# Kernel tuning notes

Hardware: AMD Instinct MI355X
Metric: run time of the kernel (lower is better)

Reference implementation:

```python
import jax, jax.numpy as jnp
import numpy as np

D_MODEL, D_STATE, EXPAND = 1024, 128, 2
E = D_MODEL * EXPAND          # 2048
N = D_STATE                   # 128
H = 1
P = E
TD = D_STATE // 2             # 64
Z_DIM = E + E + N + N + H + H + TD + H  # 4369
EPS = 1e-05
B_SZ, L = 4, 2048


def setup_inputs() -> dict:
    key = jax.random.key(0)
    ks = jax.random.split(key, 6)
    u = jax.random.normal(ks[0], (B_SZ, L, D_MODEL), dtype=jnp.float32)
    W_in = jax.random.normal(ks[1], (Z_DIM, D_MODEL), dtype=jnp.float32) * 0.02
    W_out = jax.random.normal(ks[2], (D_MODEL, E), dtype=jnp.float32) * 0.02
    w_normB = jnp.ones((N,), jnp.float32)
    w_normC = jnp.ones((N,), jnp.float32)
    B_bias = jnp.ones((N,), jnp.float32)
    C_bias = jnp.ones((N,), jnp.float32)
    # dt_bias buffer: dt_i ~ logU(0.001, 0.1); dt_bias = dt_i + log(-expm1(-dt_i))
    dt_i = jnp.exp(jax.random.uniform(ks[3], (H,)) * (np.log(0.1) - np.log(0.001)) + np.log(0.001))
    dt_i = jnp.clip(dt_i, 1e-4, None)
    dt_bias = dt_i + jnp.log(-jnp.expm1(-dt_i))
    A_log = jnp.full((H,), np.log(0.5), jnp.float32)
    return {"u": u, "W_in": W_in, "w_normB": w_normB, "w_normC": w_normC,
            "B_bias": B_bias, "C_bias": C_bias, "dt_bias": dt_bias,
            "A_log": A_log, "W_out": W_out}


def _rms(x, w):
    return x * jax.lax.rsqrt(jnp.mean(x * x, axis=-1, keepdims=True) + EPS) * w


def _rope(x, ang):
    half = x.shape[-1] // 2
    x1, x2 = x[..., :half], x[..., half:]
    c, s = jnp.cos(ang), jnp.sin(ang)
    return jnp.concatenate([x1 * c - x2 * s, x1 * s + x2 * c], axis=-1)


def reference(u, W_in, w_normB, w_normC, B_bias, C_bias, dt_bias, A_log, W_out):
    Bb, Ls, _ = u.shape
    z = u @ W_in.T  # [B, L, Z_DIM]
    o = 0
    def take(n):
        nonlocal o
        r = z[..., o:o + n]; o += n; return r
    x = jax.nn.silu(take(E))
    gate = jax.nn.silu(take(E))
    B_ = take(N)
    C_ = take(N)
    dt_ = take(H)
    A_ = take(H)
    th = take(TD)
    lam_ = take(H)

    dt = jax.nn.softplus(dt_ + dt_bias)          # [B, L, H]
    A = -jax.nn.softplus(A_ + A_log)             # [B, L, H]
    lam = jax.nn.sigmoid(lam_)                   # [B, L, H]
    alpha = jnp.exp(dt * A)                      # [B, L, H]

    B_ = _rms(B_, w_normB) + B_bias
    C_ = _rms(C_, w_normC) + C_bias
    ca = jnp.cumsum(jnp.mean(dt, axis=-1, keepdims=True) * th, axis=1)  # [B, L, TD]
    B_ = _rope(B_, ca)
    C_ = _rope(C_, ca)

    xh = x.reshape(Bb, Ls, H, P)
    xp = jnp.concatenate([jnp.zeros_like(xh[:, :1]), xh[:, :-1]], axis=1)  # roll + zero t=0
    lh = lam[..., None]
    xt = lh * xh + (1.0 - lh) * alpha[..., None] * xp  # [B, L, H, P]

    # fallback SSM: per-channel mean drive, per-head scalar A (mean over batch+time)
    u_mean = jnp.mean(xt, axis=-1)               # [B, L, H]
    A_bar = jnp.mean(A, axis=(0, 1))             # [H]
    dA = jnp.exp(dt * A_bar)                     # [B, L, H]
    dBu = dt[..., None] * B_[:, :, None, :] * u_mean[..., None]  # [B, L, H, N]

    def step(state, xs):
        dA_t, dBu_t, C_t = xs                    # [B,H], [B,H,N], [B,N]
        state = dA_t[..., None] * state + dBu_t  # [B, H, N]
        y_t = jnp.einsum('bhn,bn->bh', state, C_t)
        return state, y_t

    state0 = jnp.zeros((Bb, H, N), dtype=xt.dtype)
    _, ys = jax.lax.scan(step, state0,
                         (jnp.moveaxis(dA, 1, 0), jnp.moveaxis(dBu, 1, 0), jnp.moveaxis(C_, 1, 0)))
    outs = jnp.moveaxis(ys, 0, 1)                # [B, L, H]
    y = jnp.broadcast_to(outs, (Bb, Ls, E))      # H=1 expanded to E
    return (y * gate) @ W_out.T
```

## Files before the change

### kernel.cpp

```cpp
#include <hip/hip_runtime.h>
#include <cstdint>
#include <cstddef>

typedef __bf16 bf16_t;
typedef bf16_t bf16x8 __attribute__((ext_vector_type(8)));
typedef bf16_t bf16x4 __attribute__((ext_vector_type(4)));
typedef float f32x4 __attribute__((ext_vector_type(4)));

#define B_SZ    4
#define LSEQ    2048
#define DMODEL  1024
#define EDIM    2048
#define ZDIM    4419
#define ZPAD    4608
#define ROWS    (B_SZ*LSEQ)
#define EPSV    1e-5f

#define LDU     1088
#define LDG     2112

#define SCHUNK  128
#define SCLEN   (LSEQ/SCHUNK)
#define RCH     128
#define RCLEN   (LSEQ/RCH)

__device__ __forceinline__ float softplus_f(float x){
  return fmaxf(x, 0.f) + log1pf(expf(-fabsf(x)));
}
__device__ __forceinline__ float sigmoid_f(float x){ return 1.f/(1.f+expf(-x)); }
__device__ __forceinline__ float silu_f(float x){ return x/(1.f+expf(-x)); }

__device__ __forceinline__ void gload_lds16(const void* g, void* l){
  __builtin_amdgcn_global_load_lds(
      (const __attribute__((address_space(1))) void*)g,
      (__attribute__((address_space(3))) void*)l, 16, 0, 0);
}

__device__ __forceinline__ float blockReduce128(float v, float* red, int t){
  red[t] = v; __syncthreads();
  #pragma unroll
  for (int off = 64; off > 0; off >>= 1){
    if (t < off) red[t] += red[t+off];
    __syncthreads();
  }
  float r = red[0];
  __syncthreads();
  return r;
}

__global__ __launch_bounds__(256) void prep_kernel(
    const float4* __restrict__ u4, const float4* __restrict__ win4,
    const float4* __restrict__ wout4,
    bf16_t* __restrict__ ubf, bf16_t* __restrict__ winSh, bf16_t* __restrict__ woutSh,
    float* __restrict__ Asum, float* __restrict__ xraw)
{
  size_t i = (size_t)blockIdx.x*256 + threadIdx.x;
  if (i == 0) Asum[0] = 0.f;
  if (i < ROWS) xraw[i] = 0.f;
  const size_t NU4 = (size_t)ROWS*DMODEL/4;
  const size_t NW4 = (size_t)ZPAD*DMODEL/4;
  const size_t NO4 = (size_t)DMODEL*EDIM/4;
  if (i < NU4){
    float4 v = u4[i];
    size_t e = i*4, row = e>>10, col = e&1023;
    bf16x4 o = { (bf16_t)v.x, (bf16_t)v.y, (bf16_t)v.z, (bf16_t)v.w };
    *(bf16x4*)&ubf[row*LDU + col] = o;
    return;
  }
  i -= NU4;
  if (i < NW4){
    size_t e = i*4, row = e>>10, k = e&1023;
    bf16x4 o;
    if (row < (size_t)ZDIM){
      float4 v = win4[i];
      o = bf16x4{ (bf16_t)v.x, (bf16_t)v.y, (bf16_t)v.z, (bf16_t)v.w };
    } else {
      o = bf16x4{ (bf16_t)0.f, (bf16_t)0.f, (bf16_t)0.f, (bf16_t)0.f };
    }
    int ntile = (int)(row>>4), colf = (int)(row&15);
    int kt = (int)(k>>5), koct = (int)((k>>3)&3), ko = (int)(k&7);
    size_t off = (((size_t)ntile*32 + kt)<<9) + (koct<<7) + (colf<<3) + ko;
    *(bf16x4*)&winSh[off] = o;
    return;
  }
  i -= NW4;
  if (i < NO4){
    float4 v = wout4[i];
    size_t e = i*4, row = e>>11, k = e&2047;
    bf16x4 o = { (bf16_t)v.x, (bf16_t)v.y, (bf16_t)v.z, (bf16_t)v.w };
    int ntile = (int)(row>>4), colf = (int)(row&15);
    int kt = (int)(k>>5), koct = (int)((k>>3)&3), ko = (int)(k&7);
    size_t off = (((size_t)ntile*64 + kt)<<9) + (koct<<7) + (colf<<3) + ko;
    *(bf16x4*)&woutSh[off] = o;
  }
}

template<int LDA_, int NKT, int NT, int NXT, int MODE>
__global__ __launch_bounds__(256, 2) void gemmV_kernel(
    const bf16_t* __restrict__ A0, const bf16_t* __restrict__ Bsh,
    float* __restrict__ xraw, bf16_t* __restrict__ o_g, float* __restrict__ o_z,
    const float* __restrict__ scale, float* __restrict__ o_f)
{
  __shared__ __align__(16) bf16_t lds[8192];

  const int tid = threadIdx.x;
  const int wid = tid>>6, lane = tid&63;
  const int wr = wid>>1, wc = wid&1;
  const int lr = lane&15, hi = lane>>4;

  constexpr int MB = ROWS/128;
  constexpr int NWG = (MODE==0) ? NXT*MB : NXT*MB*2;
  const int id = blockIdx.x;
  const int rid = (id & 7)*(NWG/8) + (id>>3);
  int bx, by, kz = 0;
  if (MODE == 0){ bx = rid % NXT; by = rid / NXT; }
  else { kz = rid / (NXT*MB); int r2 = rid % (NXT*MB); bx = r2 % NXT; by = r2 / NXT; }
  const int m0 = by*128, n0 = bx*256;
  const int kt0 = kz*32;

  f32x4 acc[4][8] = {};

  const bf16_t* pA0; const bf16_t* pA1;
  int dA0, dA1;
  {
    int c0 = tid,      r0 = c0>>2, d0 = c0&3, g0 = (d0 - (r0>>1)) & 3;
    int c1 = 256+tid,  r1 = c1>>2, d1 = c1&3, g1 = (d1 - (r1>>1)) & 3;
    pA0 = A0 + (size_t)kz*1024 + (size_t)(m0+r0)*LDA_ + g0*8;
    pA1 = A0 + (size_t)kz*1024 + (size_t)(m0+r1)*LDA_ + g1*8;
    dA0 = c0*8; dA1 = c1*8;
  }
  int aoff[4];
  {
    int R0 = wr*64 + lr;
    int cA = (hi + (R0>>1)) & 3;
    #pragma unroll
    for (int m = 0; m < 4; ++m) aoff[m] = (R0 + 16*m)*32 + cA*8;
  }
  const bf16_t* bB0 = Bsh + (((size_t)((n0>>4) + wc*8)*NKT + kt0)<<9) + lane*8;
  int koff = 0;

  bf16x8 bA[8], bB[8], af[4];

  gload_lds16(pA0, &lds[dA0]); pA0 += 32;
  gload_lds16(pA1, &lds[dA1]); pA1 += 32;
  #pragma unroll
  for (int n = 0; n < 8; ++n)
    bA[n] = *(const bf16x8*)(bB0 + (size_t)n*(NKT*512) + koff);
  koff += 512;
  asm volatile("s_waitcnt vmcnt(8)" ::: "memory");
  __builtin_amdgcn_s_barrier();

  #pragma unroll 1
  for (int t2 = 0; t2 < NT/2; ++t2){
    {
      #pragma unroll
      for (int m = 0; m < 4; ++m) af[m] = *(const bf16x8*)&lds[aoff[m]];
      gload_lds16(pA0, &lds[4096 + dA0]); pA0 += 32;
      gload_lds16(pA1, &lds[4096 + dA1]); pA1 += 32;
      #pragma unroll
      for (int n = 0; n < 8; ++n)
        bB[n] = *(const bf16x8*)(bB0 + (size_t)n*(NKT*512) + koff);
      koff += 512;
      #pragma unroll
      for (int m = 0; m < 4; ++m)
        #pragma unroll
        for (int n = 0; n < 8; ++n)
          acc[m][n] = __builtin_amdgcn_mfma_f32_16x16x32_bf16(af[m], bA[n], acc[m][n], 0,0,0);
      asm volatile("s_waitcnt vmcnt(8)" ::: "memory");
      __builtin_amdgcn_s_barrier();
    }
    {
      #pragma unroll
      for (int m = 0; m < 4; ++m) af[m] = *(const bf16x8*)&lds[4096 + aoff[m]];
      const bool pf = (t2 < NT/2 - 1);
      if (pf){
        gload_lds16(pA0, &lds[dA0]); pA0 += 32;
        gload_lds16(pA1, &lds[dA1]); pA1 += 32;
        #pragma unroll
        for (int n = 0; n < 8; ++n)
          bA[n] = *(const bf16x8*)(bB0 + (size_t)n*(NKT*512) + koff);
        koff += 512;
      }
      #pragma unroll
      for (int m = 0; m < 4; ++m)
        #pragma unroll
        for (int n = 0; n < 8; ++n)
          acc[m][n] = __builtin_amdgcn_mfma_f32_16x16x32_bf16(af[m], bB[n], acc[m][n], 0,0,0);
      if (pf) { asm volatile("s_waitcnt vmcnt(8)" ::: "memory"); }
      else    { asm volatile("s_waitcnt vmcnt(0)" ::: "memory"); }
      __builtin_amdgcn_s_barrier();
    }
  }

  if (MODE == 0 && n0 < 2048){
    #pragma unroll
    for (int m = 0; m < 4; ++m){
      #pragma unroll
      for (int i = 0; i < 4; ++i){
        float p = 0.f;
        #pragma unroll
        for (int n = 0; n < 8; ++n) p += silu_f(acc[m][n][i]);
        p += __shfl_xor(p, 8); p += __shfl_xor(p, 4);
        p += __shfl_xor(p, 2); p += __shfl_xor(p, 1);
        if (lr == 0){
          int r = m0 + wr*64 + m*16 + (hi<<2) + i;
          atomicAdd(xraw + r, p);
        }
      }
    }
  } else if (MODE == 0){
    #pragma unroll
    for (int m = 0; m < 4; ++m){
      int rowb = m0 + wr*64 + m*16 + (hi<<2);
      #pragma unroll
      for (int n = 0; n < 8; ++n){
        int col = n0 + wc*128 + n*16 + lr;
        #pragma unroll
        for (int i = 0; i < 4; ++i){
          int r = rowb + i;
          float v = acc[m][n][i];
          if (col < 4096)      o_g[(size_t)r*LDG + (col-2048)] = (bf16_t)silu_f(v);
          else if (col < 4480) o_z[(size_t)r*384 + (col-4096)] = v;
        }
      }
    }
  } else {
    #pragma unroll
    for (int m = 0; m < 4; ++m){
      int rowb = m0 + wr*64 + m*16 + (hi<<2);
      #pragma unroll
      for (int i = 0; i < 4; ++i){
        int r = rowb + i;
        float s = scale[r];
        #pragma unroll
        for (int n = 0; n < 8; ++n){
          int col = n0 + wc*128 + n*16 + lr;
          atomicAdd(o_f + (size_t)r*DMODEL + col, acc[m][n][i]*s);
        }
      }
    }
  }
}

__global__ __launch_bounds__(128) void fuse_kernel(
    const float* __restrict__ xraw, const float* __restrict__ zs,
    const float* __restrict__ wnB, const float* __restrict__ wnC,
    const float* __restrict__ Bb, const float* __restrict__ Cb,
    const float* __restrict__ dtb, const float* __restrict__ Alog,
    float* __restrict__ Bn, float* __restrict__ Cn, float* __restrict__ dtth,
    float* __restrict__ dts, float* __restrict__ alphas, float* __restrict__ lams,
    float* __restrict__ xbar, float* Asum)
{
  __shared__ float red[128];
  int r = blockIdx.x, t = threadIdx.x;
  const float* zr = zs + (size_t)r*384;
  float bv = zr[t], cv = zr[128+t];
  float b2 = blockReduce128(bv*bv, red, t);
  float c2 = blockReduce128(cv*cv, red, t);
  float rb = rsqrtf(b2*(1.f/128.f) + EPSV);
  float rc = rsqrtf(c2*(1.f/128.f) + EPSV);
  Bn[(size_t)r*128 + t] = bv*rb*wnB[t] + Bb[t];
  Cn[(size_t)r*128 + t] = cv*rc*wnC[t] + Cb[t];

  float dt = softplus_f(zr[256] + dtb[0]);
  if (t < 64) dtth[(size_t)r*64 + t] = dt * zr[258+t];
  if (t == 0){
    float Av  = -softplus_f(zr[257] + Alog[0]);
    float lam = sigmoid_f(zr[322]);
    dts[r]    = dt;
    alphas[r] = expf(dt*Av);
    lams[r]   = lam;
    xbar[r]   = xraw[r] * (1.f/2048.f);
    atomicAdd(Asum, Av);
  }
}

__global__ __launch_bounds__(64) void rope_sum_kernel(
    const float* __restrict__ dtth, float* __restrict__ csum)
{
  int b  = blockIdx.x >> 7;
  int ch = blockIdx.x & 127;
  int d  = threadIdx.x;
  const float* base = dtth + ((size_t)b*LSEQ + (size_t)ch*RCLEN)*64 + d;
  float s = 0.f;
  #pragma unroll
  for (int i = 0; i < RCLEN; ++i) s += base[(size_t)i*64];
  csum[((size_t)b*RCH + ch)*64 + d] = s;
}

__global__ __launch_bounds__(64) void rope_prefix_kernel(float* __restrict__ csum)
{
  int b = blockIdx.x, d = threadIdx.x;
  float s = 0.f;
  for (int c = 0; c < RCH; ++c){
    size_t idx = ((size_t)b*RCH + c)*64 + d;
    float v = csum[idx]; csum[idx] = s; s += v;
  }
}

__global__ __launch_bounds__(64) void rope_apply_kernel(
    const float* __restrict__ dtth, const float* __restrict__ csum,
    float* __restrict__ Bn, float* __restrict__ Cn)
{
  int b  = blockIdx.x >> 7;
  int ch = blockIdx.x & 127;
  int d  = threadIdx.x;
  float ca = csum[((size_t)b*RCH + ch)*64 + d];
  int l0 = ch*RCLEN;
  const float* base = dtth + ((size_t)b*LSEQ)*64 + d;
  for (int l = l0; l < l0 + RCLEN; ++l){
    ca += base[(size_t)l*64];
    float sn, cs;
    sincosf(ca, &sn, &cs);
    size_t ro = ((size_t)b*LSEQ + l)*128;
    float b1 = Bn[ro+d], b2v = Bn[ro+64+d];
    Bn[ro+d]    = b1*cs - b2v*sn;
    Bn[ro+64+d] = b1*sn + b2v*cs;
    float c1 = Cn[ro+d], c2v = Cn[ro+64+d];
    Cn[ro+d]    = c1*cs - c2v*sn;
    Cn[ro+64+d] = c1*sn + c2v*cs;
  }
}

__global__ __launch_bounds__(64) void scan_local_kernel(
    const float* __restrict__ dts, const float* __restrict__ alphas,
    const float* __restrict__ lams, const float* __restrict__ xbar,
    const float* __restrict__ Asum,
    const float* __restrict__ Bn, const float* __restrict__ Cn,
    float* __restrict__ ylocal, float* __restrict__ Pfix,
    float* __restrict__ Sfin, float* __restrict__ Dch)
{
  int b  = blockIdx.x / SCHUNK;
  int ch = blockIdx.x % SCHUNK;
  int n  = threadIdx.x;
  float Abar = Asum[0] * (1.f/(float)ROWS);
  float s1 = 0.f, s2 = 0.f, P = 1.f;
  int l0 = ch*SCLEN;
  #pragma unroll
  for (int i = 0; i < SCLEN; ++i){
    int l = l0 + i;
    size_t r = (size_t)b*LSEQ + l;
    float dt = dts[r], lam = lams[r], al = alphas[r], xb = xbar[r];
    float xp = (l > 0) ? xbar[r-1] : 0.f;
    float um = lam*xb + (1.f-lam)*al*xp;
    float dA = expf(dt*Abar);
    float coef = dt*um;
    size_t ro = r*128;
    s1 = dA*s1 + coef*Bn[ro+n];
    s2 = dA*s2 + coef*Bn[ro+64+n];
    P *= dA;
    float p = s1*Cn[ro+n] + s2*Cn[ro+64+n];
    #pragma unroll
    for (int off = 32; off > 0; off >>= 1) p += __shfl_down(p, off);
    if (n == 0){ ylocal[r] = p; Pfix[r] = P; }
  }
  size_t so = ((size_t)b*SCHUNK + ch)*128;
  Sfin[so + n]      = s1;
  Sfin[so + 64 + n] = s2;
  if (n == 0) Dch[b*SCHUNK + ch] = P;
}

__global__ __launch_bounds__(128) void scan_carry_kernel(
    const float* __restrict__ Sfin, const float* __restrict__ Dch,
    float* __restrict__ Sin)
{
  int b = blockIdx.x;
  int n = threadIdx.x;
  float s = 0.f;
  for (int c = 0; c < SCHUNK; ++c){
    size_t so = ((size_t)b*SCHUNK + c)*128;
    Sin[so + n] = s;
    s = Dch[b*SCHUNK + c]*s + Sfin[so + n];
  }
}

__global__ __launch_bounds__(256) void scan_fix_kernel(
    const float* __restrict__ Cn, const float* __restrict__ Sin,
    const float* __restrict__ ylocal, const float* __restrict__ Pfix,
    float* __restrict__ outsv)
{
  int r = blockIdx.x*4 + (threadIdx.x>>6);
  int n = threadIdx.x & 63;
  int b  = r / LSEQ;
  int ch = (r % LSEQ) / SCLEN;
  const float* si = Sin + ((size_t)b*SCHUNK + ch)*128;
  size_t ro = (size_t)r*128;
  float p = Cn[ro+n]*si[n] + Cn[ro+64+n]*si[64+n];
  #pragma unroll
  for (int off = 32; off > 0; off >>= 1) p += __shfl_down(p, off);
  if (n == 0) outsv[r] = ylocal[r] + Pfix[r]*p;
}

extern "C" void kernel_launch(void* const* d_in, const int* in_sizes, int n_in,
                              void* d_out, int out_size, void* d_ws, size_t ws_size,
                              hipStream_t stream)
{
  const float* u    = (const float*)d_in[0];
  const float* W_in = (const float*)d_in[1];
  const float* wnB  = (const float*)d_in[2];
  const float* wnC  = (const float*)d_in[3];
  const float* Bb   = (const float*)d_in[4];
  const float* Cb   = (const float*)d_in[5];
  const float* dtb  = (const float*)d_in[6];
  const float* Alog = (const float*)d_in[7];
  const float* Wout = (const float*)d_in[8];
  float* out = (float*)d_out;
  char* ws = (char*)d_ws;

  constexpr size_t OFF_ASUM = 0;
  constexpr size_t OFF_UBF  = 256;
  constexpr size_t SZ_UBF   = (size_t)ROWS*LDU*2;
  constexpr size_t OFF_WIN  = OFF_UBF + SZ_UBF;
  constexpr size_t SZ_WIN   = (size_t)ZPAD*LDU*2;
  constexpr size_t OFF_WOUT = OFF_WIN + SZ_WIN;
  constexpr size_t SZ_WOUT  = (size_t)DMODEL*LDG*2;
  constexpr size_t OFF_G    = OFF_WOUT + SZ_WOUT;
  constexpr size_t SZ_G     = (size_t)ROWS*LDG*2;
  constexpr size_t OFF_ZS   = OFF_G + SZ_G;
  constexpr size_t SZ_ZS    = (size_t)ROWS*384*4;
  constexpr size_t OFF_BN   = OFF_ZS + SZ_ZS;
  constexpr size_t SZ_BN    = (size_t)ROWS*128*4;
  constexpr size_t OFF_CN   = OFF_BN + SZ_BN;
  constexpr size_t OFF_DTTH = OFF_CN + SZ_BN;
  constexpr size_t SZ_DTTH  = (size_t)ROWS*64*4;
  constexpr size_t OFF_XRAW = OFF_DTTH + SZ_DTTH;
  constexpr size_t OFF_DT   = OFF_XRAW + (size_t)ROWS*4;
  constexpr size_t OFF_AL   = OFF_DT  + (size_t)ROWS*4;
  constexpr size_t OFF_LAM  = OFF_AL  + (size_t)ROWS*4;
  constexpr size_t OFF_XB   = OFF_LAM + (size_t)ROWS*4;
  constexpr size_t OFF_OUTS = OFF_XB  + (size_t)ROWS*4;
  constexpr size_t OFF_YLOC = OFF_OUTS + (size_t)ROWS*4;
  constexpr size_t OFF_PFIX = OFF_YLOC + (size_t)ROWS*4;
  constexpr size_t OFF_SFIN = OFF_PFIX + (size_t)ROWS*4;
  constexpr size_t SZ_SFIN  = (size_t)B_SZ*SCHUNK*128*4;
  constexpr size_t OFF_DCH  = OFF_SFIN + SZ_SFIN;
  constexpr size_t OFF_SIN  = OFF_DCH + (size_t)B_SZ*SCHUNK*4;
  constexpr size_t OFF_CSUM = OFF_SIN + SZ_SFIN;

  float*  Asum   = (float*) (ws + OFF_ASUM);
  bf16_t* ubf    = (bf16_t*)(ws + OFF_UBF);
  bf16_t* winSh  = (bf16_t*)(ws + OFF_WIN);
  bf16_t* woutSh = (bf16_t*)(ws + OFF_WOUT);
  bf16_t* gbuf   = (bf16_t*)(ws + OFF_G);
  float*  zsb    = (float*) (ws + OFF_ZS);
  float*  Bn     = (float*) (ws + OFF_BN);
  float*  Cn     = (float*) (ws + OFF_CN);
  float*  dtth   = (float*) (ws + OFF_DTTH);
  float*  xraw   = (float*) (ws + OFF_XRAW);
  float*  dts    = (float*) (ws + OFF_DT);
  float*  alphas = (float*) (ws + OFF_AL);
  float*  lams   = (float*) (ws + OFF_LAM);
  float*  xbar   = (float*) (ws + OFF_XB);
  float*  outsv  = (float*) (ws + OFF_OUTS);
  float*  ylocal = (float*) (ws + OFF_YLOC);
  float*  Pfix   = (float*) (ws + OFF_PFIX);
  float*  Sfin   = (float*) (ws + OFF_SFIN);
  float*  Dch    = (float*) (ws + OFF_DCH);
  float*  Sin    = (float*) (ws + OFF_SIN);
  float*  csum   = (float*) (ws + OFF_CSUM);

  {
    size_t total4 = ((size_t)ROWS*DMODEL + (size_t)ZPAD*DMODEL + (size_t)DMODEL*EDIM)/4;
    int blocks = (int)((total4 + 255)/256);
    prep_kernel<<<blocks, 256, 0, stream>>>(
        (const float4*)u, (const float4*)W_in, (const float4*)Wout,
        ubf, winSh, woutSh, Asum, xraw);
  }
  hipMemsetAsync(out, 0, (size_t)ROWS*DMODEL*sizeof(float), stream);

  gemmV_kernel<LDU, 32, 32, ZPAD/256, 0>
      <<<(ZPAD/256)*(ROWS/128), 256, 0, stream>>>(
      ubf, winSh, xraw, gbuf, zsb, nullptr, nullptr);
  fuse_kernel<<<ROWS, 128, 0, stream>>>(xraw, zsb, wnB, wnC, Bb, Cb, dtb, Alog,
                                        Bn, Cn, dtth, dts, alphas, lams, xbar, Asum);
  rope_sum_kernel<<<B_SZ*RCH, 64, 0, stream>>>(dtth, csum);
  rope_prefix_kernel<<<B_SZ, 64, 0, stream>>>(csum);
  rope_apply_kernel<<<B_SZ*RCH, 64, 0, stream>>>(dtth, csum, Bn, Cn);
  scan_local_kernel<<<B_SZ*SCHUNK, 64, 0, stream>>>(dts, alphas, lams, xbar, Asum,
                                                    Bn, Cn, ylocal, Pfix, Sfin, Dch);
  scan_carry_kernel<<<B_SZ, 128, 0, stream>>>(Sfin, Dch, Sin);
  scan_fix_kernel<<<ROWS/4, 256, 0, stream>>>(Cn, Sin, ylocal, Pfix, outsv);
  gemmV_kernel<LDG, 64, 32, DMODEL/256, 1>
      <<<2*(DMODEL/256)*(ROWS/128), 256, 0, stream>>>(
      gbuf, woutSh, nullptr, nullptr, nullptr, outsv, out);
}
```

Measured before the change: 382.0 us.

## Drop split-K in output GEMM and fuse rope apply into chunked scan

```diff
diff --git a/kernel.cpp b/kernel.cpp
--- a/kernel.cpp
+++ b/kernel.cpp
@@ -109,14 +109,11 @@
   const int lr = lane&15, hi = lane>>4;
 
   constexpr int MB = ROWS/128;
-  constexpr int NWG = (MODE==0) ? NXT*MB : NXT*MB*2;
+  constexpr int NWG = NXT*MB;
   const int id = blockIdx.x;
   const int rid = (id & 7)*(NWG/8) + (id>>3);
-  int bx, by, kz = 0;
-  if (MODE == 0){ bx = rid % NXT; by = rid / NXT; }
-  else { kz = rid / (NXT*MB); int r2 = rid % (NXT*MB); bx = r2 % NXT; by = r2 / NXT; }
+  const int bx = rid % NXT, by = rid / NXT;
   const int m0 = by*128, n0 = bx*256;
-  const int kt0 = kz*32;
 
   f32x4 acc[4][8] = {};
 
@@ -125,8 +122,8 @@
   {
     int c0 = tid,      r0 = c0>>2, d0 = c0&3, g0 = (d0 - (r0>>1)) & 3;
     int c1 = 256+tid,  r1 = c1>>2, d1 = c1&3, g1 = (d1 - (r1>>1)) & 3;
-    pA0 = A0 + (size_t)kz*1024 + (size_t)(m0+r0)*LDA_ + g0*8;
-    pA1 = A0 + (size_t)kz*1024 + (size_t)(m0+r1)*LDA_ + g1*8;
+    pA0 = A0 + (size_t)(m0+r0)*LDA_ + g0*8;
+    pA1 = A0 + (size_t)(m0+r1)*LDA_ + g1*8;
     dA0 = c0*8; dA1 = c1*8;
   }
   int aoff[4];
@@ -136,7 +133,7 @@
     #pragma unroll
     for (int m = 0; m < 4; ++m) aoff[m] = (R0 + 16*m)*32 + cA*8;
   }
-  const bf16_t* bB0 = Bsh + (((size_t)((n0>>4) + wc*8)*NKT + kt0)<<9) + lane*8;
+  const bf16_t* bB0 = Bsh + (((size_t)((n0>>4) + wc*8)*NKT)<<9) + lane*8;
   int koff = 0;
 
   bf16x8 bA[8], bB[8], af[4];
@@ -235,7 +232,7 @@
         #pragma unroll
         for (int n = 0; n < 8; ++n){
           int col = n0 + wc*128 + n*16 + lr;
-          atomicAdd(o_f + (size_t)r*DMODEL + col, acc[m][n][i]*s);
+          o_f[(size_t)r*DMODEL + col] = acc[m][n][i]*s;
         }
       }
     }
@@ -298,66 +295,56 @@
   }
 }
 
-__global__ __launch_bounds__(64) void rope_apply_kernel(
+__global__ __launch_bounds__(64) void rope_scan_kernel(
     const float* __restrict__ dtth, const float* __restrict__ csum,
-    float* __restrict__ Bn, float* __restrict__ Cn)
+    const float* __restrict__ dts, const float* __restrict__ alphas,
+    const float* __restrict__ lams, const float* __restrict__ xbar,
+    const float* __restrict__ Asum,
+    const float* __restrict__ Bn, float* __restrict__ Cn,
+    float* __restrict__ ylocal, float* __restrict__ Pfix,
+    float* __restrict__ Sfin, float* __restrict__ Dch)
 {
   int b  = blockIdx.x >> 7;
   int ch = blockIdx.x & 127;
   int d  = threadIdx.x;
+  float Abar = Asum[0] * (1.f/(float)ROWS);
   float ca = csum[((size_t)b*RCH + ch)*64 + d];
-  int l0 = ch*RCLEN;
-  const float* base = dtth + ((size_t)b*LSEQ)*64 + d;
-  for (int l = l0; l < l0 + RCLEN; ++l){
-    ca += base[(size_t)l*64];
-    float sn, cs;
-    sincosf(ca, &sn, &cs);
-    size_t ro = ((size_t)b*LSEQ + l)*128;
-    float b1 = Bn[ro+d], b2v = Bn[ro+64+d];
-    Bn[ro+d]    = b1*cs - b2v*sn;
-    Bn[ro+64+d] = b1*sn + b2v*cs;
-    float c1 = Cn[ro+d], c2v = Cn[ro+64+d];
-    Cn[ro+d]    = c1*cs - c2v*sn;
-    Cn[ro+64+d] = c1*sn + c2v*cs;
-  }
-}
-
-__global__ __launch_bounds__(64) void scan_local_kernel(
-    const float* __restrict__ dts, const float* __restrict__ alphas,
-    const float* __restrict__ lams, const float* __restrict__ xbar,
-    const float* __restrict__ Asum,
-    const float* __restrict__ Bn, const float* __restrict__ Cn,
-    float* __restrict__ ylocal, float* __restrict__ Pfix,
-    float* __restrict__ Sfin, float* __restrict__ Dch)
-{
-  int b  = blockIdx.x / SCHUNK;
-  int ch = blockIdx.x % SCHUNK;
-  int n  = threadIdx.x;
-  float Abar = Asum[0] * (1.f/(float)ROWS);
   float s1 = 0.f, s2 = 0.f, P = 1.f;
   int l0 = ch*SCLEN;
   #pragma unroll
   for (int i = 0; i < SCLEN; ++i){
     int l = l0 + i;
     size_t r = (size_t)b*LSEQ + l;
+    ca += dtth[r*64 + d];
+    float sn, cs;
+    sincosf(ca, &sn, &cs);
+    size_t ro = r*128;
+    float b1 = Bn[ro+d], b2v = Bn[ro+64+d];
+    float rb1 = b1*cs - b2v*sn;
+    float rb2 = b1*sn + b2v*cs;
+    float c1 = Cn[ro+d], c2v = Cn[ro+64+d];
+    float rc1 = c1*cs - c2v*sn;
+    float rc2 = c1*sn + c2v*cs;
+    Cn[ro+d]    = rc1;
+    Cn[ro+64+d] = rc2;
+
     float dt = dts[r], lam = lams[r], al = alphas[r], xb = xbar[r];
     float xp = (l > 0) ? xbar[r-1] : 0.f;
     float um = lam*xb + (1.f-lam)*al*xp;
     float dA = expf(dt*Abar);
     float coef = dt*um;
-    size_t ro = r*128;
-    s1 = dA*s1 + coef*Bn[ro+n];
-    s2 = dA*s2 + coef*Bn[ro+64+n];
+    s1 = dA*s1 + coef*rb1;
+    s2 = dA*s2 + coef*rb2;
     P *= dA;
-    float p = s1*Cn[ro+n] + s2*Cn[ro+64+n];
+    float p = s1*rc1 + s2*rc2;
     #pragma unroll
     for (int off = 32; off > 0; off >>= 1) p += __shfl_down(p, off);
-    if (n == 0){ ylocal[r] = p; Pfix[r] = P; }
+    if (d == 0){ ylocal[r] = p; Pfix[r] = P; }
   }
   size_t so = ((size_t)b*SCHUNK + ch)*128;
-  Sfin[so + n]      = s1;
-  Sfin[so + 64 + n] = s2;
-  if (n == 0) Dch[b*SCHUNK + ch] = P;
+  Sfin[so + d]      = s1;
+  Sfin[so + 64 + d] = s2;
+  if (d == 0) Dch[b*SCHUNK + ch] = P;
 }
 
 __global__ __launch_bounds__(128) void scan_carry_kernel(
@@ -466,7 +453,6 @@
         (const float4*)u, (const float4*)W_in, (const float4*)Wout,
         ubf, winSh, woutSh, Asum, xraw);
   }
-  hipMemsetAsync(out, 0, (size_t)ROWS*DMODEL*sizeof(float), stream);
 
   gemmV_kernel<LDU, 32, 32, ZPAD/256, 0>
       <<<(ZPAD/256)*(ROWS/128), 256, 0, stream>>>(
@@ -475,12 +461,12 @@
                                         Bn, Cn, dtth, dts, alphas, lams, xbar, Asum);
   rope_sum_kernel<<<B_SZ*RCH, 64, 0, stream>>>(dtth, csum);
   rope_prefix_kernel<<<B_SZ, 64, 0, stream>>>(csum);
-  rope_apply_kernel<<<B_SZ*RCH, 64, 0, stream>>>(dtth, csum, Bn, Cn);
-  scan_local_kernel<<<B_SZ*SCHUNK, 64, 0, stream>>>(dts, alphas, lams, xbar, Asum,
-                                                    Bn, Cn, ylocal, Pfix, Sfin, Dch);
+  rope_scan_kernel<<<B_SZ*RCH, 64, 0, stream>>>(dtth, csum, dts, alphas, lams,
+                                                xbar, Asum, Bn, Cn,
+                                                ylocal, Pfix, Sfin, Dch);
   scan_carry_kernel<<<B_SZ, 128, 0, stream>>>(Sfin, Dch, Sin);
   scan_fix_kernel<<<ROWS/4, 256, 0, stream>>>(Cn, Sin, ylocal, Pfix, outsv);
-  gemmV_kernel<LDG, 64, 32, DMODEL/256, 1>
-      <<<2*(DMODEL/256)*(ROWS/128), 256, 0, stream>>>(
+  gemmV_kernel<LDG, 64, 64, DMODEL/256, 1>
+      <<<(DMODEL/256)*(ROWS/128), 256, 0, stream>>>(
       gbuf, woutSh, nullptr, nullptr, nullptr, outsv, out);
 }
```

Measured after the change: 342.8 us. 10.3% less time.
